# Optimization experiments

Hardware: AMD Instinct MI355X
Metric: run time of the kernel (lower is better)

## Reference

```python
import jax, jax.numpy as jnp
import numpy as np

N = 8192          # num nodes
E = 262144        # num edges (avg degree 32)
IN = 128          # in_channels
HID = 64          # hidden_channels
H = 4             # heads (conv1)
OUT = 16          # out_channels
THRESH = 0.5      # distance threshold for adjacency rebuild
SLOPE = 0.2       # PyG GATConv negative_slope default


def setup_inputs() -> dict:
    key = jax.random.key(0)
    ks = jax.random.split(key, 10)
    s = 0.1
    return {
        "x": jax.random.normal(ks[0], (N, IN), jnp.float32),
        "edge_index": jax.random.randint(ks[1], (2, E), 0, N, dtype=jnp.int64),
        # conv1 params (GATConv in->hid, heads=H, concat=True)
        "W1": jax.random.normal(ks[2], (IN, H * HID), jnp.float32) * s,
        "att_src1": jax.random.normal(ks[3], (H, HID), jnp.float32) * s,
        "att_dst1": jax.random.normal(ks[4], (H, HID), jnp.float32) * s,
        "b1": jax.random.normal(ks[5], (H * HID,), jnp.float32) * s,
        # conv2 params (GATConv H*hid->out, heads=1, concat=False)
        "W2": jax.random.normal(ks[6], (H * HID, OUT), jnp.float32) * s,
        "att_src2": jax.random.normal(ks[7], (OUT,), jnp.float32) * s,
        "att_dst2": jax.random.normal(ks[8], (OUT,), jnp.float32) * s,
        "b2": jax.random.normal(ks[9], (OUT,), jnp.float32) * s,
    }


def reference(x, edge_index, W1, att_src1, att_dst1, b1, W2, att_src2, att_dst2, b2):
    n = x.shape[0]
    # ---- conv1: sparse edge-wise GAT (gather -> segment-softmax -> scatter) ----
    h = (x @ W1).reshape(n, H, HID)                         # [N,H,C]
    loops = jnp.arange(n, dtype=edge_index.dtype)           # PyG adds self-loops
    src = jnp.concatenate([edge_index[0], loops])
    dst = jnp.concatenate([edge_index[1], loops])
    a_s = jnp.sum(h * att_src1, axis=-1)                    # [N,H]
    a_d = jnp.sum(h * att_dst1, axis=-1)                    # [N,H]
    e = jax.nn.leaky_relu(a_s[src] + a_d[dst], SLOPE)       # [E+N,H]
    emax = jax.ops.segment_max(e, dst, num_segments=n)      # stable softmax per dst
    ez = jnp.exp(e - emax[dst])
    denom = jax.ops.segment_sum(ez, dst, num_segments=n)
    alpha = ez / denom[dst]                                 # [E+N,H]
    agg = jax.ops.segment_sum(h[src] * alpha[..., None], dst, num_segments=n)
    h1 = jax.nn.elu(agg.reshape(n, H * HID) + b1)           # [N, H*HID]

    # ---- adjacency rebuild: pairwise Euclidean distance + threshold (detached) ----
    f = jax.lax.stop_gradient(h1)                           # torch .detach()
    sq = jnp.sum(f * f, axis=-1)                            # [N]
    d2 = sq[:, None] + sq[None, :] - 2.0 * (f @ f.T)        # squared distances
    dist = jnp.sqrt(jnp.maximum(d2, 0.0))
    adj = dist < THRESH                                     # [N,N], symmetric, self incl.

    # ---- conv2: dense masked GAT attention over rebuilt adjacency (heads=1) ----
    h2 = h1 @ W2                                            # [N,OUT]
    s2 = h2 @ att_src2                                      # [N] (source term)
    t2 = h2 @ att_dst2                                      # [N] (target term)
    # edge j->i exists iff adj[i,j]; score[i,j] = leaky_relu(a_src.h2[j] + a_dst.h2[i])
    scores = jax.nn.leaky_relu(s2[None, :] + t2[:, None], SLOPE)
    scores = jnp.where(adj, scores, -jnp.inf)
    alpha2 = jax.nn.softmax(scores, axis=1)                 # softmax over neighbors j
    out = alpha2 @ h2 + b2                                  # [N,OUT]
    return jax.nn.log_softmax(out, axis=1)
```

## Files before the change

### kernel.cpp

```cpp
#include <hip/hip_runtime.h>
#include <hip/hip_bf16.h>
#include <math.h>

#define NN 8192
#define NE 262144
#define EA (NE + NN)
#define SLOPE 0.2f
#define TH2 0.25f

typedef __bf16 bf16x8 __attribute__((ext_vector_type(8)));
typedef float f32x16 __attribute__((ext_vector_type(16)));

__device__ __forceinline__ float lrelu(float x) { return x > 0.f ? x : SLOPE * x; }

__device__ __forceinline__ void gl_lds16(const void* g, void* l) {
  __builtin_amdgcn_global_load_lds((const __attribute__((address_space(1))) void*)g,
                                   (__attribute__((address_space(3))) void*)l, 16, 0, 0);
}
__device__ __forceinline__ void gl_lds4(const void* g, void* l) {
  __builtin_amdgcn_global_load_lds((const __attribute__((address_space(1))) void*)g,
                                   (__attribute__((address_space(3))) void*)l, 4, 0, 0);
}

__global__ void k_gemm1(const float* __restrict__ x, const float* __restrict__ W1,
                        const float* __restrict__ as1, const float* __restrict__ ad1,
                        float* __restrict__ h, float* __restrict__ a_s,
                        float* __restrict__ a_d) {
  const int nb = blockIdx.x << 2;
  const int t = threadIdx.x;
  __shared__ float xs[4][128];
  if (t < 128) ((float4*)xs)[t] = ((const float4*)(x + (size_t)nb * 128))[t];
  __syncthreads();
  float ac[4] = {0.f, 0.f, 0.f, 0.f};
  const float* wp = W1 + t;
#pragma unroll 4
  for (int k = 0; k < 128; ++k) {
    float wv = wp[(size_t)k << 8];
    ac[0] = fmaf(xs[0][k], wv, ac[0]);
    ac[1] = fmaf(xs[1][k], wv, ac[1]);
    ac[2] = fmaf(xs[2][k], wv, ac[2]);
    ac[3] = fmaf(xs[3][k], wv, ac[3]);
  }
  const float as1t = as1[t], ad1t = ad1[t];
#pragma unroll
  for (int i = 0; i < 4; ++i) {
    h[((size_t)(nb + i) << 8) + t] = ac[i];
    float av = ac[i] * as1t;
    float dv = ac[i] * ad1t;
#pragma unroll
    for (int m = 32; m >= 1; m >>= 1) {
      av += __shfl_xor(av, m, 64);
      dv += __shfl_xor(dv, m, 64);
    }
    if ((t & 63) == 0) {
      a_s[((nb + i) << 2) + (t >> 6)] = av;
      a_d[((nb + i) << 2) + (t >> 6)] = dv;
    }
  }
}

__global__ void k_init(int* __restrict__ cnt) {
  int i = blockIdx.x * 256 + threadIdx.x;
  if (i < NN) cnt[i] = 1;
}
__global__ void k_hist(const int* __restrict__ ei, int* __restrict__ cnt) {
  int e = blockIdx.x * 256 + threadIdx.x;
  if (e < NE) atomicAdd(&cnt[ei[NE + e]], 1);
}
__global__ void k_scan(const int* __restrict__ cnt, int* __restrict__ start,
                       int* __restrict__ cursor) {
  __shared__ int s[1024];
  const int t = threadIdx.x;
  const int base = t << 3;
  int c[8];
  int run = 0;
#pragma unroll
  for (int i = 0; i < 8; ++i) { c[i] = cnt[base + i]; run += c[i]; }
  s[t] = run;
  __syncthreads();
  const int total = run;
  for (int off = 1; off < 1024; off <<= 1) {
    int v = (t >= off) ? s[t - off] : 0;
    __syncthreads();
    s[t] += v;
    __syncthreads();
  }
  int o = s[t] - total;
#pragma unroll
  for (int i = 0; i < 8; ++i) {
    start[base + i] = o;
    cursor[base + i] = o;
    o += c[i];
  }
}
__global__ void k_scatter(const int* __restrict__ ei, int* __restrict__ cursor,
                          int* __restrict__ eidx) {
  int e = blockIdx.x * 256 + threadIdx.x;
  if (e >= EA) return;
  int src, dst;
  if (e < NE) { src = ei[e]; dst = ei[NE + e]; } else { src = dst = e - NE; }
  int slot = atomicAdd(&cursor[dst], 1);
  eidx[slot] = src;
}

__global__ void k_node(const int* __restrict__ start, const int* __restrict__ cnt,
                       const int* __restrict__ eidx, const float* __restrict__ a_s,
                       const float* __restrict__ a_d, const float* __restrict__ h,
                       const float* __restrict__ b1, const float* __restrict__ W2,
                       const float* __restrict__ as2, const float* __restrict__ ad2,
                       __bf16* __restrict__ fbf, float* __restrict__ sq,
                       float* __restrict__ thr_g, float* __restrict__ s2_g,
                       float* __restrict__ t2g, float* __restrict__ h2g) {
  const int n = blockIdx.x, t = threadIdx.x;
  __shared__ float red[16];
  __shared__ float hl[256];
  __shared__ float r2[4];
  __shared__ float h2l[16];
  const int st = start[n];
  const int deg = cnt[n];
  const float4 ad4 = *(const float4*)(a_d + ((size_t)n << 2));
  float pm0 = -INFINITY, pm1 = -INFINITY, pm2 = -INFINITY, pm3 = -INFINITY;
  for (int e = t; e < deg; e += 256) {
    int src = eidx[st + e];
    float4 s4 = *(const float4*)(a_s + ((size_t)src << 2));
    pm0 = fmaxf(pm0, lrelu(s4.x + ad4.x));
    pm1 = fmaxf(pm1, lrelu(s4.y + ad4.y));
    pm2 = fmaxf(pm2, lrelu(s4.z + ad4.z));
    pm3 = fmaxf(pm3, lrelu(s4.w + ad4.w));
  }
#pragma unroll
  for (int m = 32; m >= 1; m >>= 1) {
    pm0 = fmaxf(pm0, __shfl_xor(pm0, m, 64));
    pm1 = fmaxf(pm1, __shfl_xor(pm1, m, 64));
    pm2 = fmaxf(pm2, __shfl_xor(pm2, m, 64));
    pm3 = fmaxf(pm3, __shfl_xor(pm3, m, 64));
  }
  if ((t & 63) == 0) {
    const int w = t >> 6;
    red[(w << 2) + 0] = pm0;
    red[(w << 2) + 1] = pm1;
    red[(w << 2) + 2] = pm2;
    red[(w << 2) + 3] = pm3;
  }
  __syncthreads();
  const int hd = t >> 6;
  const float mhead = fmaxf(fmaxf(red[0 + hd], red[4 + hd]),
                            fmaxf(red[8 + hd], red[12 + hd]));
  const float adh = (hd == 0) ? ad4.x : (hd == 1) ? ad4.y : (hd == 2) ? ad4.z : ad4.w;
  float dn0 = 0.f, dn1 = 0.f, dn2 = 0.f, dn3 = 0.f;
  float ac0 = 0.f, ac1 = 0.f, ac2 = 0.f, ac3 = 0.f;
  int e = 0;
  for (; e + 3 < deg; e += 4) {
    int s0 = eidx[st + e + 0], s1 = eidx[st + e + 1];
    int s2i = eidx[st + e + 2], s3 = eidx[st + e + 3];
    float z0 = __expf(lrelu(a_s[((size_t)s0 << 2) + hd] + adh) - mhead);
    float z1 = __expf(lrelu(a_s[((size_t)s1 << 2) + hd] + adh) - mhead);
    float z2 = __expf(lrelu(a_s[((size_t)s2i << 2) + hd] + adh) - mhead);
    float z3 = __expf(lrelu(a_s[((size_t)s3 << 2) + hd] + adh) - mhead);
    dn0 += z0; dn1 += z1; dn2 += z2; dn3 += z3;
    ac0 = fmaf(z0, h[((size_t)s0 << 8) + t], ac0);
    ac1 = fmaf(z1, h[((size_t)s1 << 8) + t], ac1);
    ac2 = fmaf(z2, h[((size_t)s2i << 8) + t], ac2);
    ac3 = fmaf(z3, h[((size_t)s3 << 8) + t], ac3);
  }
  for (; e < deg; ++e) {
    int s0 = eidx[st + e];
    float z0 = __expf(lrelu(a_s[((size_t)s0 << 2) + hd] + adh) - mhead);
    dn0 += z0;
    ac0 = fmaf(z0, h[((size_t)s0 << 8) + t], ac0);
  }
  float den = (dn0 + dn1) + (dn2 + dn3);
  float acc = (ac0 + ac1) + (ac2 + ac3);
  float v = acc / den + b1[t];
  float h1 = v > 0.f ? v : (__expf(v) - 1.f);
  fbf[((size_t)n << 8) + t] = (__bf16)h1;
  hl[t] = h1;
  float s = h1 * h1;
#pragma unroll
  for (int m = 32; m >= 1; m >>= 1) s += __shfl_xor(s, m, 64);
  if ((t & 63) == 0) r2[t >> 6] = s;
  __syncthreads();
  if (t < 16) {
    float a = 0.f;
#pragma unroll 8
    for (int c = 0; c < 256; ++c) a = fmaf(hl[c], W2[(c << 4) + t], a);
    h2g[((size_t)n << 4) + t] = a;
    h2l[t] = a;
  }
  __syncthreads();
  if (t == 0) {
    float sqv = r2[0] + r2[1] + r2[2] + r2[3];
    sq[n] = sqv;
    float ss = 0.f;
#pragma unroll
    for (int o = 0; o < 16; ++o) ss += h2l[o] * as2[o];
    thr_g[n] = (sqv - TH2) * 0.5f;
    s2_g[n] = ss;
  } else if (t == 1) {
    float tt = 0.f;
#pragma unroll
    for (int o = 0; o < 16; ++o) tt += h2l[o] * ad2[o];
    t2g[n] = tt;
  }
}

__launch_bounds__(256, 1)
__global__ void k_conv2(const __bf16* __restrict__ fbf, const float* __restrict__ sq,
                        const float* __restrict__ thr_g, const float* __restrict__ s2_g,
                        const float* __restrict__ t2g, const float* __restrict__ h2g,
                        const float* __restrict__ b2, float* __restrict__ out) {
  __shared__ __align__(16) char pool[139264];

  const int t = threadIdx.x;
  const int lane = t & 63;
  const int w = t >> 6;
  const int half = lane >> 5;
  const int lo = lane & 31;
  const int rowA = lo;
  const int i0 = blockIdx.x << 5;
  const int jw = w << 5;
  char* wbase = pool + w * 34816;

  int stoff[16];
#pragma unroll
  for (int p = 0; p < 16; ++p) {
    int rw = (p << 1) + half;
    stoff[p] = ((jw + rw) << 9) + (((lo ^ rw) & 31) << 4);
  }
  int colkey[16];
#pragma unroll
  for (int kc = 0; kc < 16; ++kc)
    colkey[kc] = ((((kc << 1) + half) ^ rowA) & 31) << 4;

  bf16x8 bfr[16];
  {
    const char* fb = (const char*)fbf + (((size_t)(i0 + rowA)) << 9) + (half << 4);
#pragma unroll
    for (int kc = 0; kc < 16; ++kc) bfr[kc] = *(const bf16x8*)(fb + kc * 32);
  }
  const float sqi = sq[i0 + rowA];
  const float t2i = t2g[i0 + rowA];
  const float gb_i = 0.5f * sqi;

  float m = -INFINITY, l = 0.f;
  float o[16];
#pragma unroll
  for (int c = 0; c < 16; ++c) o[c] = 0.f;

#define STAGE(B, JT)                                                        \
  do {                                                                      \
    const char* gsrc = (const char*)fbf + ((size_t)(JT) << 16);             \
    char* lb_ = wbase + (B)*17408;                                          \
    _Pragma("unroll") for (int p = 0; p < 16; ++p)                          \
        gl_lds16(gsrc + stoff[p], lb_ + (p << 10));                         \
    gl_lds4(thr_g + ((JT) << 7) + lane, lb_ + 16384);                       \
    gl_lds4(thr_g + ((JT) << 7) + 64 + lane, lb_ + 16384 + 256);            \
    gl_lds4(s2_g + ((JT) << 7) + lane, lb_ + 16896);                        \
    gl_lds4(s2_g + ((JT) << 7) + 64 + lane, lb_ + 16896 + 256);             \
  } while (0)

  STAGE(0, 0);

  for (int jt = 0; jt < 64; ++jt) {
    const int cur = jt & 1;
    if (jt < 63) {
      STAGE(cur ^ 1, jt + 1);
      asm volatile("s_waitcnt vmcnt(20)" ::: "memory");
    } else {
      asm volatile("s_waitcnt vmcnt(0)" ::: "memory");
    }
    char* lb = wbase + cur * 17408;
    const char* rb = lb + (rowA << 9);

    f32x16 acc0, acc1;
#pragma unroll
    for (int r = 0; r < 16; ++r) { acc0[r] = 0.f; acc1[r] = 0.f; }
#pragma unroll
    for (int kc = 0; kc < 16; kc += 2) {
      bf16x8 a0 = *(const bf16x8*)(rb + colkey[kc]);
      bf16x8 a1 = *(const bf16x8*)(rb + colkey[kc + 1]);
      acc0 = __builtin_amdgcn_mfma_f32_32x32x16_bf16(a0, bfr[kc], acc0, 0, 0, 0);
      acc1 = __builtin_amdgcn_mfma_f32_32x32x16_bf16(a1, bfr[kc + 1], acc1, 0, 0, 0);
    }

    const float* thp = (const float*)(lb + 16384);
    const float* s2p = (const float*)(lb + 16896);
    float4 thq[4], s2q[4];
#pragma unroll
    for (int q = 0; q < 4; ++q) {
      thq[q] = *(const float4*)(thp + jw + (half << 2) + (q << 3));
      s2q[q] = *(const float4*)(s2p + jw + (half << 2) + (q << 3));
    }
    const float thv[16] = {thq[0].x, thq[0].y, thq[0].z, thq[0].w,
                           thq[1].x, thq[1].y, thq[1].z, thq[1].w,
                           thq[2].x, thq[2].y, thq[2].z, thq[2].w,
                           thq[3].x, thq[3].y, thq[3].z, thq[3].w};
    const float s2v[16] = {s2q[0].x, s2q[0].y, s2q[0].z, s2q[0].w,
                           s2q[1].x, s2q[1].y, s2q[1].z, s2q[1].w,
                           s2q[2].x, s2q[2].y, s2q[2].z, s2q[2].w,
                           s2q[3].x, s2q[3].y, s2q[3].z, s2q[3].w};

    unsigned msk = 0;
#pragma unroll
    for (int r = 0; r < 16; ++r) {
      float g = acc0[r] + acc1[r];
      if (g > gb_i + thv[r]) msk |= (1u << r);
    }

    if (msk) {
      const int j0 = (jt << 7) + jw + (half << 2);
#pragma unroll
      for (int r = 0; r < 16; ++r) {
        if (msk & (1u << r)) {
          float e = lrelu(s2v[r] + t2i);
          if (e > m) {
            float scl = __expf(m - e);
            l *= scl;
#pragma unroll
            for (int c = 0; c < 16; ++c) o[c] *= scl;
            m = e;
          }
          float p = __expf(e - m);
          l += p;
          int j = j0 + (r & 3) + ((r >> 2) << 3);
          const float4* hp = (const float4*)(h2g + ((size_t)j << 4));
          float4 q0 = hp[0], q1 = hp[1], q2 = hp[2], q3 = hp[3];
          o[0] += p * q0.x;  o[1] += p * q0.y;  o[2] += p * q0.z;  o[3] += p * q0.w;
          o[4] += p * q1.x;  o[5] += p * q1.y;  o[6] += p * q1.z;  o[7] += p * q1.w;
          o[8] += p * q2.x;  o[9] += p * q2.y;  o[10] += p * q2.z; o[11] += p * q2.w;
          o[12] += p * q3.x; o[13] += p * q3.y; o[14] += p * q3.z; o[15] += p * q3.w;
        }
      }
    }
  }

  __syncthreads();
  float (*mrg)[18] = (float(*)[18])pool;
  {
    float* mp = mrg[t];
    mp[0] = m;
    mp[1] = l;
#pragma unroll
    for (int c = 0; c < 16; ++c) mp[2 + c] = o[c];
  }
  __syncthreads();
  if (t < 32) {
    float M = -INFINITY;
#pragma unroll
    for (int s = 0; s < 8; ++s)
      M = fmaxf(M, mrg[((s >> 1) << 6) + ((s & 1) << 5) + t][0]);
    float L = 0.f, O[16];
#pragma unroll
    for (int c = 0; c < 16; ++c) O[c] = 0.f;
#pragma unroll
    for (int s = 0; s < 8; ++s) {
      const float* mp = mrg[((s >> 1) << 6) + ((s & 1) << 5) + t];
      float wt = __expf(mp[0] - M);
      L += mp[1] * wt;
#pragma unroll
      for (int c = 0; c < 16; ++c) O[c] += mp[2 + c] * wt;
    }
    float inv = 1.f / L;
    float v[16];
    float mx = -INFINITY;
#pragma unroll
    for (int c = 0; c < 16; ++c) {
      v[c] = O[c] * inv + b2[c];
      mx = fmaxf(mx, v[c]);
    }
    float se = 0.f;
#pragma unroll
    for (int c = 0; c < 16; ++c) se += __expf(v[c] - mx);
    float lse = mx + __logf(se);
    float4* op = (float4*)(out + ((size_t)(i0 + t) << 4));
#pragma unroll
    for (int gq = 0; gq < 4; ++gq)
      op[gq] = make_float4(v[gq * 4 + 0] - lse, v[gq * 4 + 1] - lse,
                           v[gq * 4 + 2] - lse, v[gq * 4 + 3] - lse);
  }
#undef STAGE
}

extern "C" void kernel_launch(void* const* d_in, const int* in_sizes, int n_in,
                              void* d_out, int out_size, void* d_ws, size_t ws_size,
                              hipStream_t stream) {
  const float* x   = (const float*)d_in[0];
  const int*   ei  = (const int*)d_in[1];
  const float* W1  = (const float*)d_in[2];
  const float* as1 = (const float*)d_in[3];
  const float* ad1 = (const float*)d_in[4];
  const float* b1  = (const float*)d_in[5];
  const float* W2  = (const float*)d_in[6];
  const float* as2 = (const float*)d_in[7];
  const float* ad2 = (const float*)d_in[8];
  const float* b2  = (const float*)d_in[9];
  float* out = (float*)d_out;

  float* p = (float*)d_ws;
  float* h     = p; p += (size_t)NN * 256;
  float* a_s   = p; p += (size_t)NN * 4;
  float* a_d   = p; p += (size_t)NN * 4;
  float* sq    = p; p += NN;
  float* t2    = p; p += NN;
  float* h2g   = p; p += (size_t)NN * 16;
  float* thr_g = p; p += NN;
  float* s2_g  = p; p += NN;
  __bf16* fbf  = (__bf16*)p; p += (size_t)NN * 128;
  int* cnt     = (int*)p; p += NN;
  int* startp  = (int*)p; p += NN;
  int* cursor  = (int*)p; p += NN;
  int* eidx    = (int*)p;

  k_init<<<NN / 256, 256, 0, stream>>>(cnt);
  k_hist<<<NE / 256, 256, 0, stream>>>(ei, cnt);
  k_gemm1<<<NN / 4, 256, 0, stream>>>(x, W1, as1, ad1, h, a_s, a_d);
  k_scan<<<1, 1024, 0, stream>>>(cnt, startp, cursor);
  k_scatter<<<(EA + 255) / 256, 256, 0, stream>>>(ei, cursor, eidx);
  k_node<<<NN, 256, 0, stream>>>(startp, cnt, eidx, a_s, a_d, h, b1, W2, as2, ad2,
                                 fbf, sq, thr_g, s2_g, t2, h2g);
  k_conv2<<<NN / 32, 256, 0, stream>>>(fbf, sq, thr_g, s2_g, t2, h2g, b2, out);
}
```

Measured before the change: 261.4 us.

## Drop LDS staging in conv2 and load tiles directly with more waves

The dense masked-attention kernel no longer stages feature tiles and threshold/score vectors through LDS with async global-to-LDS copies and double buffering. Each wave now loads its 32-row bf16 A fragments and per-column scalars straight from global memory into registers. The block grows to 512 threads with two blocks per CU, so each wave covers half as many column tiles. The change relies on extra waves and cache hits to hide load latency, but it gives up the explicit prefetch pipeline and issues strided 16-byte loads per lane.

Result: slower. 310.6 us (+18.8%).

```diff
diff --git a/kernel.cpp b/kernel.cpp
--- a/kernel.cpp
+++ b/kernel.cpp
@@ -12,15 +12,6 @@
 typedef float f32x16 __attribute__((ext_vector_type(16)));
 
 __device__ __forceinline__ float lrelu(float x) { return x > 0.f ? x : SLOPE * x; }
-
-__device__ __forceinline__ void gl_lds16(const void* g, void* l) {
-  __builtin_amdgcn_global_load_lds((const __attribute__((address_space(1))) void*)g,
-                                   (__attribute__((address_space(3))) void*)l, 16, 0, 0);
-}
-__device__ __forceinline__ void gl_lds4(const void* g, void* l) {
-  __builtin_amdgcn_global_load_lds((const __attribute__((address_space(1))) void*)g,
-                                   (__attribute__((address_space(3))) void*)l, 4, 0, 0);
-}
 
 __global__ void k_gemm1(const float* __restrict__ x, const float* __restrict__ W1,
                         const float* __restrict__ as1, const float* __restrict__ ad1,
@@ -204,33 +195,20 @@
   }
 }
 
-__launch_bounds__(256, 1)
+__launch_bounds__(512, 2)
 __global__ void k_conv2(const __bf16* __restrict__ fbf, const float* __restrict__ sq,
                         const float* __restrict__ thr_g, const float* __restrict__ s2_g,
                         const float* __restrict__ t2g, const float* __restrict__ h2g,
                         const float* __restrict__ b2, float* __restrict__ out) {
-  __shared__ __align__(16) char pool[139264];
+  __shared__ float mrg[512][18];
 
   const int t = threadIdx.x;
   const int lane = t & 63;
   const int w = t >> 6;
   const int half = lane >> 5;
-  const int lo = lane & 31;
-  const int rowA = lo;
+  const int rowA = lane & 31;
   const int i0 = blockIdx.x << 5;
   const int jw = w << 5;
-  char* wbase = pool + w * 34816;
-
-  int stoff[16];
-#pragma unroll
-  for (int p = 0; p < 16; ++p) {
-    int rw = (p << 1) + half;
-    stoff[p] = ((jw + rw) << 9) + (((lo ^ rw) & 31) << 4);
-  }
-  int colkey[16];
-#pragma unroll
-  for (int kc = 0; kc < 16; ++kc)
-    colkey[kc] = ((((kc << 1) + half) ^ rowA) & 31) << 4;
 
   bf16x8 bfr[16];
   {
@@ -247,49 +225,30 @@
 #pragma unroll
   for (int c = 0; c < 16; ++c) o[c] = 0.f;
 
-#define STAGE(B, JT)                                                        \
-  do {                                                                      \
-    const char* gsrc = (const char*)fbf + ((size_t)(JT) << 16);             \
-    char* lb_ = wbase + (B)*17408;                                          \
-    _Pragma("unroll") for (int p = 0; p < 16; ++p)                          \
-        gl_lds16(gsrc + stoff[p], lb_ + (p << 10));                         \
-    gl_lds4(thr_g + ((JT) << 7) + lane, lb_ + 16384);                       \
-    gl_lds4(thr_g + ((JT) << 7) + 64 + lane, lb_ + 16384 + 256);            \
-    gl_lds4(s2_g + ((JT) << 7) + lane, lb_ + 16896);                        \
-    gl_lds4(s2_g + ((JT) << 7) + 64 + lane, lb_ + 16896 + 256);             \
-  } while (0)
-
-  STAGE(0, 0);
-
-  for (int jt = 0; jt < 64; ++jt) {
-    const int cur = jt & 1;
-    if (jt < 63) {
-      STAGE(cur ^ 1, jt + 1);
-      asm volatile("s_waitcnt vmcnt(20)" ::: "memory");
-    } else {
-      asm volatile("s_waitcnt vmcnt(0)" ::: "memory");
-    }
-    char* lb = wbase + cur * 17408;
-    const char* rb = lb + (rowA << 9);
-
+  for (int jt = 0; jt < 32; ++jt) {
+    const int jbase = (jt << 8) + jw;
+    bf16x8 afr[16];
+    {
+      const char* fr = (const char*)fbf + ((size_t)(jbase + rowA) << 9) + (half << 4);
+#pragma unroll
+      for (int kc = 0; kc < 16; ++kc) afr[kc] = *(const bf16x8*)(fr + kc * 32);
+    }
     f32x16 acc0, acc1;
 #pragma unroll
     for (int r = 0; r < 16; ++r) { acc0[r] = 0.f; acc1[r] = 0.f; }
 #pragma unroll
     for (int kc = 0; kc < 16; kc += 2) {
-      bf16x8 a0 = *(const bf16x8*)(rb + colkey[kc]);
-      bf16x8 a1 = *(const bf16x8*)(rb + colkey[kc + 1]);
-      acc0 = __builtin_amdgcn_mfma_f32_32x32x16_bf16(a0, bfr[kc], acc0, 0, 0, 0);
-      acc1 = __builtin_amdgcn_mfma_f32_32x32x16_bf16(a1, bfr[kc + 1], acc1, 0, 0, 0);
-    }
-
-    const float* thp = (const float*)(lb + 16384);
-    const float* s2p = (const float*)(lb + 16896);
+      acc0 = __builtin_amdgcn_mfma_f32_32x32x16_bf16(afr[kc], bfr[kc], acc0, 0, 0, 0);
+      acc1 = __builtin_amdgcn_mfma_f32_32x32x16_bf16(afr[kc + 1], bfr[kc + 1], acc1, 0, 0, 0);
+    }
+
+    const float* tb = thr_g + jbase + (half << 2);
+    const float* sb = s2_g + jbase + (half << 2);
     float4 thq[4], s2q[4];
 #pragma unroll
     for (int q = 0; q < 4; ++q) {
-      thq[q] = *(const float4*)(thp + jw + (half << 2) + (q << 3));
-      s2q[q] = *(const float4*)(s2p + jw + (half << 2) + (q << 3));
+      thq[q] = *(const float4*)(tb + (q << 3));
+      s2q[q] = *(const float4*)(sb + (q << 3));
     }
     const float thv[16] = {thq[0].x, thq[0].y, thq[0].z, thq[0].w,
                            thq[1].x, thq[1].y, thq[1].z, thq[1].w,
@@ -308,7 +267,7 @@
     }
 
     if (msk) {
-      const int j0 = (jt << 7) + jw + (half << 2);
+      const int j0 = jbase + (half << 2);
 #pragma unroll
       for (int r = 0; r < 16; ++r) {
         if (msk & (1u << r)) {
@@ -334,10 +293,8 @@
     }
   }
 
-  __syncthreads();
-  float (*mrg)[18] = (float(*)[18])pool;
   {
-    float* mp = mrg[t];
+    float* mp = mrg[(w << 6) + (half << 5) + rowA];
     mp[0] = m;
     mp[1] = l;
 #pragma unroll
@@ -347,13 +304,13 @@
   if (t < 32) {
     float M = -INFINITY;
 #pragma unroll
-    for (int s = 0; s < 8; ++s)
+    for (int s = 0; s < 16; ++s)
       M = fmaxf(M, mrg[((s >> 1) << 6) + ((s & 1) << 5) + t][0]);
     float L = 0.f, O[16];
 #pragma unroll
     for (int c = 0; c < 16; ++c) O[c] = 0.f;
 #pragma unroll
-    for (int s = 0; s < 8; ++s) {
+    for (int s = 0; s < 16; ++s) {
       const float* mp = mrg[((s >> 1) << 6) + ((s & 1) << 5) + t];
       float wt = __expf(mp[0] - M);
       L += mp[1] * wt;
@@ -378,7 +335,6 @@
       op[gq] = make_float4(v[gq * 4 + 0] - lse, v[gq * 4 + 1] - lse,
                            v[gq * 4 + 2] - lse, v[gq * 4 + 3] - lse);
   }
-#undef STAGE
 }
 
 extern "C" void kernel_launch(void* const* d_in, const int* in_sizes, int n_in,
@@ -418,5 +374,5 @@
   k_scatter<<<(EA + 255) / 256, 256, 0, stream>>>(ei, cursor, eidx);
   k_node<<<NN, 256, 0, stream>>>(startp, cnt, eidx, a_s, a_d, h, b1, W2, as2, ad2,
                                  fbf, sq, thr_g, s2_g, t2, h2g);
-  k_conv2<<<NN / 32, 256, 0, stream>>>(fbf, sq, thr_g, s2_g, t2, h2g, b2, out);
-}
+  k_conv2<<<NN / 32, 512, 0, stream>>>(fbf, sq, thr_g, s2_g, t2, h2g, b2, out);
+}
```
